# Kernel optimization log

Measured on AMD Instinct MI355X. Metric: run time of the kernel, lower is better.

The kernel has to match this reference:

```python
import jax, jax.numpy as jnp
import numpy as np

EPSILON = 1e-6
MINMAX_RATIO = 20 ** 0.5
N_NODES, N_EDGES = 60000, 240000
WIDTH, NUM_HEAD, DIM_HEAD = 256, 8, 32
WIDTH_NORM = NUM_HEAD * DIM_HEAD          # 256
WIDTH_ACT = NUM_HEAD * DIM_HEAD * 4       # 1024
EDGE_VOCAB, EDGE_FEATS = 16, 3


def _inv_softplus(y):
    return np.log(np.expm1(y))


def setup_inputs() -> dict:
    key = jax.random.key(0)
    ks = jax.random.split(key, 16)
    inp = {
        'x': jax.random.normal(ks[0], (N_NODES, WIDTH), jnp.float32),
        'deg': jax.random.randint(ks[1], (N_NODES,), 0, 6, jnp.int32),
        'edge_idx': jax.random.randint(ks[2], (2, N_EDGES), 0, N_NODES, jnp.int32),
        'edge_attr': jax.random.randint(ks[3], (N_EDGES, EDGE_FEATS), 0, EDGE_VOCAB, jnp.int32),
        'node_elec': jax.random.normal(ks[4], (N_NODES, 2), jnp.float32),
        # parameters (init scales per module code)
        'lora_down': jax.random.normal(ks[5], (WIDTH, DIM_HEAD)) / np.sqrt(WIDTH),
        # original init is zeros; small random values used so this path is exercised
        'lora_up': jax.random.normal(ks[6], (DIM_HEAD, WIDTH_NORM)) * 0.01,
        'emb_edge': jax.random.normal(ks[7], (EDGE_VOCAB, DIM_HEAD)) * (0.01 / np.sqrt(EDGE_FEATS)),
        'moa_w': jnp.zeros((2, DIM_HEAD), jnp.float32),
        'moa_s': jnp.tile(jnp.linspace(float(_inv_softplus(0.1)), float(_inv_softplus(10.0)), DIM_HEAD), (2, 1)),
        'elec_lin': jax.random.normal(ks[8], (2, DIM_HEAD)) * (0.01 / np.sqrt(2)),
        'emb_deg': jax.random.normal(ks[9], (6, WIDTH_NORM)) * 0.1,
        'lin_pre': jax.random.normal(ks[10], (WIDTH, WIDTH_NORM)) / np.sqrt(WIDTH),
        'gate_lin': jax.random.normal(ks[11], (WIDTH_NORM, WIDTH_NORM)) / np.sqrt(WIDTH_NORM),
        'gate_kernel': jax.random.normal(ks[12], (NUM_HEAD, DIM_HEAD, DIM_HEAD * 4)) / np.sqrt(DIM_HEAD),
        'value_lin': jax.random.normal(ks[13], (WIDTH_NORM, WIDTH_NORM)) / np.sqrt(WIDTH_NORM),
        'value_kernel': jax.random.normal(ks[14], (NUM_HEAD, DIM_HEAD, DIM_HEAD * 4)) / np.sqrt(DIM_HEAD),
        'act_bias': jnp.full((WIDTH_ACT,), float(_inv_softplus(0.5)), jnp.float32),
        'post_kernel': jax.random.normal(ks[15], (NUM_HEAD, DIM_HEAD * 4, DIM_HEAD)) / np.sqrt(DIM_HEAD * 4),
    }
    return inp


def _clip_with_grad(x, lo, hi):
    return jax.lax.stop_gradient(jnp.clip(x, lo, hi) - x) + x


def _group_linear(x, lin_kernel, head_kernel, norm_bias=None):
    H, D, F = head_kernel.shape
    xx = (x @ lin_kernel).reshape(*x.shape[:-1], H, D)
    xx = xx / jnp.sqrt(jnp.mean(jnp.square(xx), axis=-1, keepdims=True) + EPSILON)
    if norm_bias is not None:
        xx = (xx + norm_bias.reshape(xx.shape)) / 2 ** 0.5
    xx = jnp.einsum('nhd,hdf->nhf', xx, head_kernel)
    return xx.reshape(*x.shape[:-1], H * F)


def reference(x, deg, edge_idx, edge_attr, node_elec, lora_down, lora_up, emb_edge,
              moa_w, moa_s, elec_lin, emb_deg, lin_pre, gate_lin, gate_kernel,
              value_lin, value_kernel, act_bias, post_kernel):
    ei0, ei1 = edge_idx[0], edge_idx[1]
    # edge embedding: bond features + electronegativity difference (MoAct tanh mixture)
    diff = node_elec[ei0] - node_elec[ei1]                      # [E,2]
    w = jax.nn.softplus(moa_w)
    w = w / w.sum(axis=-1, keepdims=True)
    s = jax.nn.softplus(moa_s)
    moa_out = (jnp.tanh(diff[..., None] * s) * w).sum(-1)       # [E,2]
    emb = jnp.sum(emb_edge[edge_attr], axis=-2) + moa_out @ elec_lin  # [E,dim_head]
    # per-edge message with LoRA modulation, scatter-add to destination nodes
    msg = x[ei0] + x[ei1]                                       # [E,width]
    msg = msg @ lin_pre + ((msg @ lora_down) * emb) @ lora_up   # [E,width_norm]
    agg = jax.ops.segment_sum(msg, ei1, num_segments=x.shape[0])
    # gated post-block with degree-embedding gate bias
    gate_bias = emb_deg[deg]                                    # [N,width_norm]
    gg = _group_linear(agg, gate_lin, gate_kernel, gate_bias)   # [N,width_act]
    vv = _group_linear(agg, value_lin, value_kernel)
    a = jax.nn.softplus(gg + act_bias)
    a = _clip_with_grad(a, 1.0 / MINMAX_RATIO, MINMAX_RATIO)
    xx = (a * vv).reshape(agg.shape[0], NUM_HEAD, -1)           # [N,H,4*dim_head]
    xx = jnp.einsum('nhd,hdf->nhf', xx, post_kernel)
    return xx.reshape(agg.shape[0], -1)                         # [N,width_norm]
```

## Files before the change

kernel.cpp:

```cpp
#include <hip/hip_runtime.h>
#include <hip/hip_bf16.h>

typedef unsigned short u16;

#define NN 60000
#define NE 240000

typedef __attribute__((ext_vector_type(8))) short bfrag;
typedef __attribute__((ext_vector_type(4))) float ffrag;

__device__ __forceinline__ float bf2f(u16 u) {
    union { unsigned int i; float f; } v; v.i = ((unsigned int)u) << 16; return v.f;
}
__device__ __forceinline__ u16 f2bf(float f) {
    __hip_bfloat16 h = __float2bfloat16(f);
    return *reinterpret_cast<u16*>(&h);
}
__device__ __forceinline__ float softplusf(float x) {
    return fmaxf(x, 0.f) + log1pf(expf(-fabsf(x)));
}
__device__ __forceinline__ float fast_softplus(float x) {
    return __logf(1.f + __expf(x));
}
__device__ __forceinline__ float fast_sp_clip(float x) {
    float a = __logf(1.f + __expf(x));
    return fminf(fmaxf(a, 0.22360679774997896f), 4.47213595499957939f);
}
__device__ __forceinline__ float fast_tanh(float x) {
    float t = __expf(fminf(fmaxf(2.f * x, -30.f), 30.f));
    return (t - 1.f) * __builtin_amdgcn_rcpf(t + 1.f);
}
template<bool B>
__device__ __forceinline__ float LD(const void* p, int i) {
    if constexpr (B) return bf2f(((const u16*)p)[i]);
    else             return ((const float*)p)[i];
}
__device__ __forceinline__ bfrag ldfrag(const u16* p) {
    return *reinterpret_cast<const bfrag*>(p);
}
__device__ __forceinline__ ffrag MFMA(bfrag a, bfrag b, ffrag c) {
    return __builtin_amdgcn_mfma_f32_16x16x32_bf16(a, b, c, 0, 0, 0);
}

__global__ void detect_kernel(const u16* __restrict__ x, int* __restrict__ flag) {
    __shared__ int cnt;
    if (threadIdx.x == 0) cnt = 0;
    __syncthreads();
    int c = 0;
    for (int i = threadIdx.x; i < 2048; i += 256) {
        u16 w = x[2 * i];
        int e = (w >> 7) & 0xFF;
        if (e >= 112 && e <= 143) c++;
    }
    atomicAdd(&cnt, c);
    __syncthreads();
    if (threadIdx.x == 0) *flag = (cnt > 1024) ? 1 : 0;
}

template<bool B>
__device__ void prep_body(const void* gate_lin, const void* value_lin,
    const void* lin_pre, const void* lora_down, const void* lora_up,
    const void* gate_kernel, const void* value_kernel, const void* post_kernel,
    u16* gT, u16* vT, u16* lpT, u16* ldT, u16* luT, u16* gkT, u16* vkT, u16* pkT,
    int tid, int stride)
{
    for (int i = tid; i < 65536; i += stride) {
        int n = i >> 8, k = i & 255;
        gT[i]  = f2bf(LD<B>(gate_lin,  k * 256 + n));
        vT[i]  = f2bf(LD<B>(value_lin, k * 256 + n));
        lpT[i] = f2bf(LD<B>(lin_pre,   k * 256 + n));
    }
    for (int i = tid; i < 8192; i += stride) {
        { int n = i >> 8, k = i & 255; ldT[i] = f2bf(LD<B>(lora_down, k * 32 + n)); }
        { int n = i >> 5, k = i & 31;  luT[i] = f2bf(LD<B>(lora_up,   k * 256 + n)); }
    }
    for (int i = tid; i < 32768; i += stride) {
        { int hf = i >> 5, d = i & 31, h = hf >> 7, f = hf & 127;
          gkT[i] = f2bf(LD<B>(gate_kernel,  h * 4096 + d * 128 + f));
          vkT[i] = f2bf(LD<B>(value_kernel, h * 4096 + d * 128 + f)); }
        { int hd = i >> 7, f = i & 127, h = hd >> 5, d2 = hd & 31;
          pkT[i] = f2bf(LD<B>(post_kernel, h * 4096 + f * 32 + d2)); }
    }
}
__global__ void prep_kernel(const void* gate_lin, const void* value_lin,
    const void* lin_pre, const void* lora_down, const void* lora_up,
    const void* gate_kernel, const void* value_kernel, const void* post_kernel,
    u16* gT, u16* vT, u16* lpT, u16* ldT, u16* luT, u16* gkT, u16* vkT, u16* pkT,
    const int* flag)
{
    int tid = blockIdx.x * blockDim.x + threadIdx.x;
    int stride = gridDim.x * blockDim.x;
    if (*flag) prep_body<true >(gate_lin, value_lin, lin_pre, lora_down, lora_up,
        gate_kernel, value_kernel, post_kernel, gT, vT, lpT, ldT, luT, gkT, vkT, pkT, tid, stride);
    else       prep_body<false>(gate_lin, value_lin, lin_pre, lora_down, lora_up,
        gate_kernel, value_kernel, post_kernel, gT, vT, lpT, ldT, luT, gkT, vkT, pkT, tid, stride);
}


struct PreSmem { __align__(16) u16 xB[64][264]; };

template<bool B>
__device__ void pre_body(PreSmem& sm, const void* x, const u16* ldT,
                         u16* xb, u16* xd, int blk, int j)
{
    const int w = j >> 6, quad = (j >> 4) & 3, l15 = j & 15;
    {
        int row = j >> 2, seg = j & 3, c0 = seg * 64;
        int gr = blk * 64 + row;
        if (gr < NN) {
            if constexpr (B) {
                const u16* xp = (const u16*)x + (size_t)gr * 256 + c0;
                for (int cc = 0; cc < 64; cc += 8)
                    *reinterpret_cast<bfrag*>(&sm.xB[row][c0 + cc]) = ldfrag(xp + cc);
            } else {
                const float* xp = (const float*)x + (size_t)gr * 256 + c0;
                u16* xbp = xb + (size_t)gr * 256 + c0;
                for (int cc = 0; cc < 64; cc += 8) {
                    float4 v0 = *(const float4*)(xp + cc);
                    float4 v1 = *(const float4*)(xp + cc + 4);
                    bfrag o;
                    o[0] = (short)f2bf(v0.x); o[1] = (short)f2bf(v0.y);
                    o[2] = (short)f2bf(v0.z); o[3] = (short)f2bf(v0.w);
                    o[4] = (short)f2bf(v1.x); o[5] = (short)f2bf(v1.y);
                    o[6] = (short)f2bf(v1.z); o[7] = (short)f2bf(v1.w);
                    *reinterpret_cast<bfrag*>(&sm.xB[row][c0 + cc]) = o;
                    *reinterpret_cast<bfrag*>(xbp + cc) = o;
                }
            }
        } else {
            bfrag z = {0,0,0,0,0,0,0,0};
            for (int cc = 0; cc < 64; cc += 8)
                *reinterpret_cast<bfrag*>(&sm.xB[row][c0 + cc]) = z;
        }
    }
    __syncthreads();
    const int r0 = w * 16;
    bfrag A[8];
    #pragma unroll
    for (int kt = 0; kt < 8; kt++)
        A[kt] = ldfrag(&sm.xB[r0 + l15][kt * 32 + quad * 8]);

    #pragma unroll
    for (int t = 0; t < 2; t++) {
        int n0 = t * 16;
        ffrag acc = {0.f, 0.f, 0.f, 0.f};
        #pragma unroll
        for (int kt = 0; kt < 8; kt++)
            acc = MFMA(A[kt], ldfrag(ldT + (n0 + l15) * 256 + kt * 32 + quad * 8), acc);
        #pragma unroll
        for (int r = 0; r < 4; r++) {
            int gr = blk * 64 + r0 + quad * 4 + r;
            if (gr < NN) xd[(size_t)gr * 32 + n0 + l15] = f2bf(acc[r]);
        }
    }
}
__global__ __launch_bounds__(256) void pre_kernel(const void* x, const u16* ldT,
    u16* xb, u16* xd, const int* flag)
{
    __shared__ PreSmem sm;
    const int j = threadIdx.x, blk = blockIdx.x;
    if (*flag) pre_body<true >(sm, x, ldT, xb, xd, blk, j);
    else       pre_body<false>(sm, x, ldT, xb, xd, blk, j);
}

__global__ __launch_bounds__(256) void hist_kernel(const int* __restrict__ edge_idx,
                                                   int* __restrict__ cnt)
{
    int e = blockIdx.x * blockDim.x + threadIdx.x;
    int stride = gridDim.x * blockDim.x;
    for (; e < NE; e += stride) atomicAdd(&cnt[edge_idx[NE + e]], 1);
}

__global__ __launch_bounds__(256) void scanA_kernel(const int* __restrict__ cnt,
                                                    int* __restrict__ bsum)
{
    __shared__ int sd[256];
    int b = blockIdx.x, j = threadIdx.x;
    int base = b * 1024 + j * 4;
    int s = 0;
    #pragma unroll
    for (int k = 0; k < 4; k++) { int i = base + k; if (i < NN) s += cnt[i]; }
    sd[j] = s; __syncthreads();
    for (int st = 128; st > 0; st >>= 1) {
        if (j < st) sd[j] += sd[j + st];
        __syncthreads();
    }
    if (j == 0) bsum[b] = sd[0];
}

__global__ __launch_bounds__(256) void scanB_kernel(const int* __restrict__ cnt,
    const int* __restrict__ bsum, int* __restrict__ off, int* __restrict__ cur)
{
    __shared__ int sd[256];
    int b = blockIdx.x, j = threadIdx.x;
    int pre = 0;
    for (int k = 0; k < b; k++) pre += bsum[k];
    int base = b * 1024 + j * 4;
    int c[4]; int tsum = 0;
    #pragma unroll
    for (int k = 0; k < 4; k++) { int i = base + k; c[k] = (i < NN) ? cnt[i] : 0; tsum += c[k]; }
    sd[j] = tsum; __syncthreads();
    for (int st = 1; st < 256; st <<= 1) {
        int v = (j >= st) ? sd[j - st] : 0;
        __syncthreads();
        sd[j] += v;
        __syncthreads();
    }
    int excl = sd[j] - tsum;
    int run = pre + excl;
    #pragma unroll
    for (int k = 0; k < 4; k++) {
        int i = base + k;
        if (i < NN) { off[i] = run; cur[i] = run; }
        run += c[k];
    }
}

struct EdgeWSmem {
    float wL[64], sL[64];
    float embT[512];
    float elT[64];
};

template<bool B>
__device__ void edgew_body(EdgeWSmem& sm, const int* edge_idx, const int* edge_attr,
    const void* node_elec, const void* emb_edge, const void* moa_w, const void* moa_s,
    const void* elec_lin, const u16* xd, u16* W, int* srcL, int* cur, int g, int j)
{
    if (j < 64) {
        int c = j >> 5;
        float sw = fast_softplus(LD<B>(moa_w, j));
        float tot = 0.f;
        #pragma unroll
        for (int d = 0; d < 32; d++) tot += fast_softplus(LD<B>(moa_w, c * 32 + d));
        sm.wL[j] = sw / tot;
        sm.sL[j] = fast_softplus(LD<B>(moa_s, j));
        sm.elT[j] = LD<B>(elec_lin, j);
    }
    for (int i = j; i < 512; i += 256) sm.embT[i] = LD<B>(emb_edge, i);
    __syncthreads();

    const int t = j & 3, s = j >> 2, e = g * 64 + s;
    const int a = edge_idx[e], b = edge_idx[NE + e];
    const int ch = t >> 1, dr = (t & 1) * 16;
    float df = LD<B>(node_elec, a * 2 + ch) - LD<B>(node_elec, b * 2 + ch);
    float part = 0.f;
    #pragma unroll
    for (int d = 0; d < 16; d++) {
        int dd = ch * 32 + dr + d;
        part += fast_tanh(df * sm.sL[dd]) * sm.wL[dd];
    }
    part += __shfl_xor(part, 1);
    int base = (j & 63) & ~3;
    float moa0 = __shfl(part, base + 0);
    float moa1 = __shfl(part, base + 2);

    int a0 = edge_attr[e * 3 + 0], a1 = edge_attr[e * 3 + 1], a2 = edge_attr[e * 3 + 2];
    int d0 = t * 8;
    bfrag va = ldfrag(xd + (size_t)a * 32 + d0);
    bfrag vb = ldfrag(xd + (size_t)b * 32 + d0);
    bfrag o;
    #pragma unroll
    for (int q = 0; q < 8; q++) {
        int d = d0 + q;
        float emb = sm.embT[a0 * 32 + d] + sm.embT[a1 * 32 + d] + sm.embT[a2 * 32 + d]
                  + moa0 * sm.elT[d] + moa1 * sm.elT[32 + d];
        o[q] = (short)f2bf((bf2f((u16)va[q]) + bf2f((u16)vb[q])) * emb);
    }
    int slot = 0;
    if (t == 0) slot = atomicAdd(&cur[b], 1);
    slot = __shfl(slot, base);
    if (t == 0) srcL[slot] = a;
    *reinterpret_cast<bfrag*>(W + (size_t)slot * 32 + d0) = o;
}

__global__ __launch_bounds__(256) void edgew_kernel(const int* edge_idx,
    const int* edge_attr, const void* node_elec, const void* emb_edge,
    const void* moa_w, const void* moa_s, const void* elec_lin,
    const u16* xd, u16* W, int* srcL, int* cur, const int* flag)
{
    __shared__ EdgeWSmem sm;
    const int j = threadIdx.x, g = blockIdx.x;
    if (*flag) edgew_body<true >(sm, edge_idx, edge_attr, node_elec, emb_edge,
                                 moa_w, moa_s, elec_lin, xd, W, srcL, cur, g, j);
    else       edgew_body<false>(sm, edge_idx, edge_attr, node_elec, emb_edge,
                                 moa_w, moa_s, elec_lin, xd, W, srcL, cur, g, j);
}

struct NodeSmemF {
    __align__(16) union U1 {
        u16 aggB[16][264];
        u16 ghatB[16][264];
    } u1;
    __align__(16) union U2 {
        struct P { float gF[16][260]; float vF[16][260]; } p;
        u16 xxB[16][1032];
    } u2;
    __align__(16) u16 sB[16][264];
    __align__(16) u16 uB[16][40];
    float grmsL[16][8], vrmsL[16][8];
    int degL[16], offL[16], idgL[16];
    int srcC[128];
};

template<bool B>
__device__ void node_body_f(NodeSmemF& sm, const void* x, const u16* xb,
    const u16* Wb, const int* srcL, const int* off, const int* cnt, const int* deg,
    const void* emb_deg, const void* act_bias, const u16* gT, const u16* vT,
    const u16* gkT, const u16* vkT, const u16* pkT, const u16* lpT, const u16* luT,
    void* out, int blk, int j)
{
    const int w = j >> 6, quad = (j >> 4) & 3, l15 = j & 15;
    const int n0g = blk * 16;
    const u16* xbp = B ? (const u16*)x : xb;

    int o0 = off[n0g];
    int eb = off[n0g + 15] + cnt[n0g + 15] - o0;
    if (j < 128 && j < eb) sm.srcC[j] = srcL[o0 + j];
    if (j < 16) {
        sm.degL[j] = deg[n0g + j];
        sm.offL[j] = off[n0g + j];
        sm.idgL[j] = cnt[n0g + j];
    }
    __syncthreads();

    {
        int s = j >> 4, dp = j & 15, c0 = dp * 16;
        int o = sm.offL[s], dg = sm.idgL[s], base = o - o0;
        float acc[16];
        #pragma unroll
        for (int k = 0; k < 16; k++) acc[k] = 0.f;
        float u0 = 0.f, u1 = 0.f;
        for (int i = 0; i < dg; i++) {
            int idx = base + i;
            int src = (idx < 128) ? sm.srcC[idx] : srcL[o + i];
            const u16* xr = xbp + (size_t)src * 256 + c0;
            bfrag v0 = ldfrag(xr), v1 = ldfrag(xr + 8);
            const u16* wr = Wb + (size_t)(o + i) * 32 + dp;
            u0 += bf2f(wr[0]); u1 += bf2f(wr[16]);
            #pragma unroll
            for (int q = 0; q < 8; q++) {
                acc[q]     += bf2f((u16)v0[q]);
                acc[q + 8] += bf2f((u16)v1[q]);
            }
        }
        {
            const u16* xr = xbp + (size_t)(n0g + s) * 256 + c0;
            bfrag v0 = ldfrag(xr), v1 = ldfrag(xr + 8);
            float fd = (float)dg;
            #pragma unroll
            for (int q = 0; q < 8; q++) {
                acc[q]     = fmaf(fd, bf2f((u16)v0[q]), acc[q]);
                acc[q + 8] = fmaf(fd, bf2f((u16)v1[q]), acc[q + 8]);
            }
        }
        sm.uB[s][dp] = f2bf(u0); sm.uB[s][dp + 16] = f2bf(u1);
        #pragma unroll
        for (int cq = 0; cq < 16; cq += 2) {
            unsigned int pv = (unsigned int)f2bf(acc[cq]) | ((unsigned int)f2bf(acc[cq + 1]) << 16);
            *reinterpret_cast<unsigned int*>(&sm.sB[s][c0 + cq]) = pv;
        }
    }
    __syncthreads();

    {
        bfrag S[8];
        #pragma unroll
        for (int kt = 0; kt < 8; kt++)
            S[kt] = ldfrag(&sm.sB[l15][kt * 32 + quad * 8]);
        bfrag uA = ldfrag(&sm.uB[l15][quad * 8]);
        #pragma unroll
        for (int tt = 0; tt < 4; tt++) {
            int n0 = (w * 4 + tt) * 16;
            const u16* bp = lpT + (n0 + l15) * 256 + quad * 8;
            bfrag b0 = ldfrag(bp +   0), b1 = ldfrag(bp +  32),
                  b2 = ldfrag(bp +  64), b3 = ldfrag(bp +  96),
                  b4 = ldfrag(bp + 128), b5 = ldfrag(bp + 160),
                  b6 = ldfrag(bp + 192), b7 = ldfrag(bp + 224);
            bfrag lu = ldfrag(luT + (n0 + l15) * 32 + quad * 8);
            ffrag acc = {0.f, 0.f, 0.f, 0.f};
            acc = MFMA(S[0], b0, acc); acc = MFMA(S[1], b1, acc);
            acc = MFMA(S[2], b2, acc); acc = MFMA(S[3], b3, acc);
            acc = MFMA(S[4], b4, acc); acc = MFMA(S[5], b5, acc);
            acc = MFMA(S[6], b6, acc); acc = MFMA(S[7], b7, acc);
            acc = MFMA(uA, lu, acc);
            #pragma unroll
            for (int r = 0; r < 4; r++)
                sm.u1.aggB[quad * 4 + r][n0 + l15] = f2bf(acc[r]);
        }
    }
    __syncthreads();

    {
        bfrag A[8];
        #pragma unroll
        for (int kt = 0; kt < 8; kt++)
            A[kt] = ldfrag(&sm.u1.aggB[l15][kt * 32 + quad * 8]);
        const u16* WT = (w >> 1) ? vT : gT;
        float (*OF)[260] = (w >> 1) ? sm.u2.p.vF : sm.u2.p.gF;
        int half = (w & 1) * 128;
        #pragma unroll
        for (int t = 0; t < 8; t++) {
            int n0 = half + t * 16;
            const u16* bp = WT + (n0 + l15) * 256 + quad * 8;
            bfrag b0 = ldfrag(bp +   0), b1 = ldfrag(bp +  32),
                  b2 = ldfrag(bp +  64), b3 = ldfrag(bp +  96),
                  b4 = ldfrag(bp + 128), b5 = ldfrag(bp + 160),
                  b6 = ldfrag(bp + 192), b7 = ldfrag(bp + 224);
            ffrag acc = {0.f, 0.f, 0.f, 0.f};
            acc = MFMA(A[0], b0, acc); acc = MFMA(A[1], b1, acc);
            acc = MFMA(A[2], b2, acc); acc = MFMA(A[3], b3, acc);
            acc = MFMA(A[4], b4, acc); acc = MFMA(A[5], b5, acc);
            acc = MFMA(A[6], b6, acc); acc = MFMA(A[7], b7, acc);
            #pragma unroll
            for (int r = 0; r < 4; r++)
                OF[quad * 4 + r][n0 + l15] = acc[r];
        }
    }
    __syncthreads();

    if (j < 128) {
        int r = j >> 3, h = j & 7;
        float gs = 0.f, vs = 0.f;
        #pragma unroll
        for (int d = 0; d < 32; d++) {
            float g = sm.u2.p.gF[r][h * 32 + d]; gs = fmaf(g, g, gs);
            float v = sm.u2.p.vF[r][h * 32 + d]; vs = fmaf(v, v, vs);
        }
        sm.grmsL[r][h] = 1.f / sqrtf(gs * (1.f / 32.f) + 1e-6f);
        sm.vrmsL[r][h] = 1.f / sqrtf(vs * (1.f / 32.f) + 1e-6f);
    }
    __syncthreads();

    {
        int row = j >> 4, c0 = l15 * 16;
        int dg = sm.degL[row];
        float bias[16];
        if constexpr (B) {
            const u16* ep = (const u16*)emb_deg + dg * 256 + c0;
            bfrag e0 = ldfrag(ep), e1 = ldfrag(ep + 8);
            #pragma unroll
            for (int q = 0; q < 8; q++) {
                bias[q] = bf2f((u16)e0[q]); bias[q + 8] = bf2f((u16)e1[q]);
            }
        } else {
            const float* ep = (const float*)emb_deg + dg * 256 + c0;
            #pragma unroll
            for (int q = 0; q < 16; q += 4) {
                float4 v = *(const float4*)(ep + q);
                bias[q] = v.x; bias[q + 1] = v.y; bias[q + 2] = v.z; bias[q + 3] = v.w;
            }
        }
        float gi = sm.grmsL[row][c0 >> 5], vi = sm.vrmsL[row][c0 >> 5];
        #pragma unroll
        for (int cq = 0; cq < 16; cq += 2) {
            int c = c0 + cq;
            float v0 = sm.u2.p.vF[row][c] * vi;
            float v1 = sm.u2.p.vF[row][c + 1] * vi;
            float g0 = (sm.u2.p.gF[row][c] * gi + bias[cq]) * 0.70710678118654752f;
            float g1 = (sm.u2.p.gF[row][c + 1] * gi + bias[cq + 1]) * 0.70710678118654752f;
            unsigned int pv = (unsigned int)f2bf(v0) | ((unsigned int)f2bf(v1) << 16);
            unsigned int pg = (unsigned int)f2bf(g0) | ((unsigned int)f2bf(g1) << 16);
            *reinterpret_cast<unsigned int*>(&sm.sB[row][c]) = pv;
            *reinterpret_cast<unsigned int*>(&sm.u1.ghatB[row][c]) = pg;
        }
    }
    __syncthreads();

    #pragma unroll
    for (int hh = 0; hh < 2; hh++) {
        int h = w * 2 + hh;
        bfrag aG = ldfrag(&sm.u1.ghatB[l15][h * 32 + quad * 8]);
        bfrag aV = ldfrag(&sm.sB[l15][h * 32 + quad * 8]);
        #pragma unroll
        for (int t = 0; t < 8; t++) {
            int n0 = t * 16;
            bfrag bg = ldfrag(gkT + (h * 128 + n0 + l15) * 32 + quad * 8);
            bfrag bv = ldfrag(vkT + (h * 128 + n0 + l15) * 32 + quad * 8);
            ffrag zero = {0.f, 0.f, 0.f, 0.f};
            ffrag ag = MFMA(aG, bg, zero);
            ffrag av = MFMA(aV, bv, zero);
            int cc = h * 128 + n0 + l15;
            float bias = LD<B>(act_bias, cc);
            #pragma unroll
            for (int r = 0; r < 4; r++) {
                float a = fast_sp_clip(ag[r] + bias);
                sm.u2.xxB[quad * 4 + r][cc] = f2bf(a * av[r]);
            }
        }
    }
    __syncthreads();

    #pragma unroll
    for (int hh = 0; hh < 2; hh++) {
        int h = w * 2 + hh;
        bfrag A4[4];
        #pragma unroll
        for (int kt = 0; kt < 4; kt++)
            A4[kt] = ldfrag(&sm.u2.xxB[l15][h * 128 + kt * 32 + quad * 8]);
        #pragma unroll
        for (int t = 0; t < 2; t++) {
            int n0 = t * 16;
            const u16* pp = pkT + (h * 32 + n0 + l15) * 128 + quad * 8;
            bfrag c0 = ldfrag(pp), c1 = ldfrag(pp + 32),
                  c2 = ldfrag(pp + 64), c3 = ldfrag(pp + 96);
            ffrag acc = {0.f, 0.f, 0.f, 0.f};
            acc = MFMA(A4[0], c0, acc); acc = MFMA(A4[1], c1, acc);
            acc = MFMA(A4[2], c2, acc); acc = MFMA(A4[3], c3, acc);
            #pragma unroll
            for (int r = 0; r < 4; r++) {
                size_t idx = (size_t)(n0g + quad * 4 + r) * 256 + h * 32 + n0 + l15;
                if constexpr (B) ((u16*)out)[idx] = f2bf(acc[r]);
                else             ((float*)out)[idx] = acc[r];
            }
        }
    }
}

__global__ __launch_bounds__(256) void node_kernel_f(
    const void* x, const u16* xb, const u16* Wb, const int* srcL, const int* off,
    const int* cnt, const int* deg, const void* emb_deg, const void* act_bias,
    const u16* gT, const u16* vT, const u16* gkT, const u16* vkT, const u16* pkT,
    const u16* lpT, const u16* luT, void* out, const int* flag)
{
    __shared__ NodeSmemF sm;
    const int j = threadIdx.x, blk = blockIdx.x;
    if (*flag) node_body_f<true >(sm, x, xb, Wb, srcL, off, cnt, deg, emb_deg, act_bias,
                                  gT, vT, gkT, vkT, pkT, lpT, luT, out, blk, j);
    else       node_body_f<false>(sm, x, xb, Wb, srcL, off, cnt, deg, emb_deg, act_bias,
                                  gT, vT, gkT, vkT, pkT, lpT, luT, out, blk, j);
}

struct EdgeSmemM {
    __align__(16) u16 msgB[64][264];
    __align__(16) u16 uB[64][40];
    __align__(16) float embL[64][32];
    float wL[64], sL[64];
    float moaL[64][2];
    int ei0s[64], ei1s[64];
};

template<bool B>
__device__ void edge_body_m(EdgeSmemM& sm, const void* x, const int* edge_idx,
    const int* edge_attr, const void* node_elec, const void* emb_edge,
    const void* moa_w, const void* moa_s, const void* elec_lin,
    const u16* ldT, const u16* luT, const u16* lpT, float* agg, int g, int j)
{
    const int w = j >> 6, quad = (j >> 4) & 3, l15 = j & 15;
    const int lane = j & 63;

    if (w == 0) {
        int c = lane >> 5;
        float sw = softplusf(LD<B>(moa_w, lane));
        float tot = 0.f;
        #pragma unroll
        for (int d = 0; d < 32; d++) tot += softplusf(LD<B>(moa_w, c * 32 + d));
        sm.wL[lane] = sw / tot;
        sm.sL[lane] = softplusf(LD<B>(moa_s, lane));
        int e = g * 64 + lane;
        int a = edge_idx[e], b = edge_idx[NE + e];
        sm.ei0s[lane] = a; sm.ei1s[lane] = b;
        #pragma unroll
        for (int c2 = 0; c2 < 2; c2++) {
            float df = LD<B>(node_elec, a * 2 + c2) - LD<B>(node_elec, b * 2 + c2);
            float acc = 0.f;
            for (int d = 0; d < 32; d++)
                acc += tanhf(df * sm.sL[c2 * 32 + d]) * sm.wL[c2 * 32 + d];
            sm.moaL[lane][c2] = acc;
        }
    }
    __syncthreads();

    {
        int row = j >> 2, seg = j & 3, c0 = seg * 64;
        int e0 = sm.ei0s[row], e1 = sm.ei1s[row];
        if constexpr (B) {
            const u16* xp = (const u16*)x;
            for (int cc = 0; cc < 64; cc += 8) {
                bfrag v0 = ldfrag(xp + (size_t)e0 * 256 + c0 + cc);
                bfrag v1 = ldfrag(xp + (size_t)e1 * 256 + c0 + cc);
                bfrag o;
                #pragma unroll
                for (int q = 0; q < 8; q++)
                    o[q] = (short)f2bf(bf2f((u16)v0[q]) + bf2f((u16)v1[q]));
                *reinterpret_cast<bfrag*>(&sm.msgB[row][c0 + cc]) = o;
            }
        } else {
            const float* xp = (const float*)x;
            for (int cc = 0; cc < 64; cc += 4) {
                float4 v0 = *(const float4*)(xp + (size_t)e0 * 256 + c0 + cc);
                float4 v1 = *(const float4*)(xp + (size_t)e1 * 256 + c0 + cc);
                ushort4 o = { f2bf(v0.x + v1.x), f2bf(v0.y + v1.y),
                              f2bf(v0.z + v1.z), f2bf(v0.w + v1.w) };
                *reinterpret_cast<ushort4*>(&sm.msgB[row][c0 + cc]) = o;
            }
        }
        int e = row, d0 = seg * 8, ea = g * 64 + e;
        int a0 = edge_attr[ea * 3 + 0], a1 = edge_attr[ea * 3 + 1], a2 = edge_attr[ea * 3 + 2];
        float m0 = sm.moaL[e][0], m1 = sm.moaL[e][1];
        #pragma unroll
        for (int d = d0; d < d0 + 8; d++) {
            sm.embL[e][d] = LD<B>(emb_edge, a0 * 32 + d) + LD<B>(emb_edge, a1 * 32 + d)
                          + LD<B>(emb_edge, a2 * 32 + d)
                          + m0 * LD<B>(elec_lin, d) + m1 * LD<B>(elec_lin, 32 + d);
        }
    }
    __syncthreads();

    const int r0 = w * 16;
    bfrag A[8];
    #pragma unroll
    for (int kt = 0; kt < 8; kt++)
        A[kt] = ldfrag(&sm.msgB[r0 + l15][kt * 32 + quad * 8]);

    #pragma unroll
    for (int t = 0; t < 2; t++) {
        int n0 = t * 16;
        ffrag acc = {0.f, 0.f, 0.f, 0.f};
        #pragma unroll
        for (int kt = 0; kt < 8; kt++)
            acc = MFMA(A[kt], ldfrag(ldT + (n0 + l15) * 256 + kt * 32 + quad * 8), acc);
        #pragma unroll
        for (int r = 0; r < 4; r++) {
            int row = r0 + quad * 4 + r;
            sm.uB[row][n0 + l15] = f2bf(acc[r] * sm.embL[row][n0 + l15]);
        }
    }
    bfrag uA = ldfrag(&sm.uB[r0 + l15][quad * 8]);

    int er[4];
    #pragma unroll
    for (int r = 0; r < 4; r++) er[r] = sm.ei1s[r0 + quad * 4 + r];

    for (int t = 0; t < 16; t++) {
        int n0 = t * 16;
        ffrag acc = {0.f, 0.f, 0.f, 0.f};
        #pragma unroll
        for (int kt = 0; kt < 8; kt++)
            acc = MFMA(A[kt], ldfrag(lpT + (n0 + l15) * 256 + kt * 32 + quad * 8), acc);
        acc = MFMA(uA, ldfrag(luT + (n0 + l15) * 32 + quad * 8), acc);
        #pragma unroll
        for (int r = 0; r < 4; r++)
            unsafeAtomicAdd(&agg[(size_t)er[r] * 256 + n0 + l15], acc[r]);
    }
}

__global__ __launch_bounds__(256) void edge_kernel_m(
    const void* x, const int* edge_idx, const int* edge_attr,
    const void* node_elec, const void* emb_edge, const void* moa_w,
    const void* moa_s, const void* elec_lin,
    const u16* ldT, const u16* luT, const u16* lpT, float* agg, const int* flag)
{
    __shared__ EdgeSmemM sm;
    const int j = threadIdx.x, g = blockIdx.x;
    if (*flag) edge_body_m<true >(sm, x, edge_idx, edge_attr, node_elec, emb_edge,
                                  moa_w, moa_s, elec_lin, ldT, luT, lpT, agg, g, j);
    else       edge_body_m<false>(sm, x, edge_idx, edge_attr, node_elec, emb_edge,
                                  moa_w, moa_s, elec_lin, ldT, luT, lpT, agg, g, j);
}

struct NodeSmemM {
    union U1 {
        u16 aggB[16][264];
        u16 ghatB[16][264];
    } u1;
    union U2 {
        struct P { float gF[16][260]; float vF[16][260]; } p;
        u16 xxB[16][1032];
    } u2;
    __align__(16) u16 vhatB[16][264];
    float grmsL[16][8], vrmsL[16][8];
    int degL[16];
};

template<bool B>
__device__ void node_body_m(NodeSmemM& sm, const float* agg, const int* deg,
    const void* emb_deg, const void* act_bias, const u16* gT, const u16* vT,
    const u16* gkT, const u16* vkT, const u16* pkT, void* out, int blk, int j)
{
    const int w = j >> 6, quad = (j >> 4) & 3, l15 = j & 15;
    const int n0g = blk * 16;

    {
        int row = j >> 4, c0 = l15 * 16;
        const float* ap = agg + (size_t)(n0g + row) * 256 + c0;
        #pragma unroll
        for (int q = 0; q < 16; q += 4) {
            float4 v = *(const float4*)(ap + q);
            ushort4 o = { f2bf(v.x), f2bf(v.y), f2bf(v.z), f2bf(v.w) };
            *reinterpret_cast<ushort4*>(&sm.u1.aggB[row][c0 + q]) = o;
        }
        if (j < 16) sm.degL[j] = deg[n0g + j];
    }
    __syncthreads();

    {
        bfrag A[8];
        #pragma unroll
        for (int kt = 0; kt < 8; kt++)
            A[kt] = ldfrag(&sm.u1.aggB[l15][kt * 32 + quad * 8]);
        const u16* WT = (w >> 1) ? vT : gT;
        float (*OF)[260] = (w >> 1) ? sm.u2.p.vF : sm.u2.p.gF;
        int half = (w & 1) * 128;
        #pragma unroll
        for (int t = 0; t < 8; t++) {
            int n0 = half + t * 16;
            ffrag acc = {0.f, 0.f, 0.f, 0.f};
            #pragma unroll
            for (int kt = 0; kt < 8; kt++)
                acc = MFMA(A[kt], ldfrag(WT + (n0 + l15) * 256 + kt * 32 + quad * 8), acc);
            #pragma unroll
            for (int r = 0; r < 4; r++)
                OF[quad * 4 + r][n0 + l15] = acc[r];
        }
    }
    __syncthreads();

    if (j < 128) {
        int r = j >> 3, h = j & 7;
        float gs = 0.f, vs = 0.f;
        #pragma unroll
        for (int d = 0; d < 32; d++) {
            float g = sm.u2.p.gF[r][h * 32 + d]; gs = fmaf(g, g, gs);
            float v = sm.u2.p.vF[r][h * 32 + d]; vs = fmaf(v, v, vs);
        }
        sm.grmsL[r][h] = 1.f / sqrtf(gs * (1.f / 32.f) + 1e-6f);
        sm.vrmsL[r][h] = 1.f / sqrtf(vs * (1.f / 32.f) + 1e-6f);
    }
    __syncthreads();

    {
        int row = j >> 4, c0 = l15 * 16;
        int dg = sm.degL[row];
        #pragma unroll
        for (int c = c0; c < c0 + 16; c++) {
            float gi = sm.grmsL[row][c >> 5], vi = sm.vrmsL[row][c >> 5];
            float bias = LD<B>(emb_deg, dg * 256 + c);
            sm.vhatB[row][c] = f2bf(sm.u2.p.vF[row][c] * vi);
            sm.u1.ghatB[row][c] = f2bf((sm.u2.p.gF[row][c] * gi + bias) * 0.70710678118654752f);
        }
    }
    __syncthreads();

    #pragma unroll
    for (int hh = 0; hh < 2; hh++) {
        int h = w * 2 + hh;
        bfrag aG = ldfrag(&sm.u1.ghatB[l15][h * 32 + quad * 8]);
        bfrag aV = ldfrag(&sm.vhatB[l15][h * 32 + quad * 8]);
        #pragma unroll
        for (int t = 0; t < 8; t++) {
            int n0 = t * 16;
            ffrag zero = {0.f, 0.f, 0.f, 0.f};
            ffrag ag = MFMA(aG, ldfrag(gkT + (h * 128 + n0 + l15) * 32 + quad * 8), zero);
            ffrag av = MFMA(aV, ldfrag(vkT + (h * 128 + n0 + l15) * 32 + quad * 8), zero);
            int cc = h * 128 + n0 + l15;
            float bias = LD<B>(act_bias, cc);
            #pragma unroll
            for (int r = 0; r < 4; r++) {
                float a = softplusf(ag[r] + bias);
                a = fminf(fmaxf(a, 0.22360679774997896f), 4.47213595499957939f);
                sm.u2.xxB[quad * 4 + r][cc] = f2bf(a * av[r]);
            }
        }
    }
    __syncthreads();

    #pragma unroll
    for (int hh = 0; hh < 2; hh++) {
        int h = w * 2 + hh;
        bfrag A4[4];
        #pragma unroll
        for (int kt = 0; kt < 4; kt++)
            A4[kt] = ldfrag(&sm.u2.xxB[l15][h * 128 + kt * 32 + quad * 8]);
        #pragma unroll
        for (int t = 0; t < 2; t++) {
            int n0 = t * 16;
            ffrag acc = {0.f, 0.f, 0.f, 0.f};
            #pragma unroll
            for (int kt = 0; kt < 4; kt++)
                acc = MFMA(A4[kt], ldfrag(pkT + (h * 32 + n0 + l15) * 128 + kt * 32 + quad * 8), acc);
            #pragma unroll
            for (int r = 0; r < 4; r++) {
                size_t idx = (size_t)(n0g + quad * 4 + r) * 256 + h * 32 + n0 + l15;
                if constexpr (B) ((u16*)out)[idx] = f2bf(acc[r]);
                else             ((float*)out)[idx] = acc[r];
            }
        }
    }
}

__global__ __launch_bounds__(256) void node_kernel_m(
    const float* agg, const int* deg, const void* emb_deg, const void* act_bias,
    const u16* gT, const u16* vT, const u16* gkT, const u16* vkT, const u16* pkT,
    void* out, const int* flag)
{
    __shared__ NodeSmemM sm;
    const int j = threadIdx.x, blk = blockIdx.x;
    if (*flag) node_body_m<true >(sm, agg, deg, emb_deg, act_bias, gT, vT, gkT, vkT, pkT, out, blk, j);
    else       node_body_m<false>(sm, agg, deg, emb_deg, act_bias, gT, vT, gkT, vkT, pkT, out, blk, j);
}

struct EdgeSmemFB {
    __align__(16) float msgT[256][8];
    __align__(16) float uT[32][8];
    float wL[64], sL[64];
    float embL[8][32];
    float moaL[8][2];
    float diffL[8][2];
    int   ei0s[8], ei1s[8];
};

template<bool B>
__device__ void edge_body_fb(EdgeSmemFB& sm,
    const void* x, const int* edge_idx, const int* edge_attr,
    const void* node_elec, const void* lora_down, const void* lora_up,
    const void* emb_edge, const void* moa_w, const void* moa_s,
    const void* elec_lin, const void* lin_pre, float* agg, int g, int j)
{
    if (j < 64) {
        int c = j >> 5;
        float sw = softplusf(LD<B>(moa_w, j));
        float tot = 0.f;
        #pragma unroll
        for (int d = 0; d < 32; d++) tot += softplusf(LD<B>(moa_w, c * 32 + d));
        sm.wL[j] = sw / tot;
        sm.sL[j] = softplusf(LD<B>(moa_s, j));
    }
    if (j < 16) {
        int s = j >> 1, c = j & 1;
        int e = g * 8 + s;
        int a = edge_idx[e], b = edge_idx[NE + e];
        if (c == 0) { sm.ei0s[s] = a; sm.ei1s[s] = b; }
        sm.diffL[s][c] = LD<B>(node_elec, a * 2 + c) - LD<B>(node_elec, b * 2 + c);
    }
    __syncthreads();
    if (j < 16) {
        int s = j >> 1, c = j & 1;
        float df = sm.diffL[s][c], acc = 0.f;
        #pragma unroll
        for (int d = 0; d < 32; d++)
            acc += tanhf(df * sm.sL[c * 32 + d]) * sm.wL[c * 32 + d];
        sm.moaL[s][c] = acc;
    }
    #pragma unroll
    for (int s = 0; s < 8; s++)
        sm.msgT[j][s] = LD<B>(x, sm.ei0s[s] * 256 + j) + LD<B>(x, sm.ei1s[s] * 256 + j);
    __syncthreads();
    {
        int s = j >> 5, d = j & 31, e = g * 8 + s;
        sm.embL[s][d] = LD<B>(emb_edge, edge_attr[e * 3 + 0] * 32 + d)
                      + LD<B>(emb_edge, edge_attr[e * 3 + 1] * 32 + d)
                      + LD<B>(emb_edge, edge_attr[e * 3 + 2] * 32 + d)
                      + sm.moaL[s][0] * LD<B>(elec_lin, d)
                      + sm.moaL[s][1] * LD<B>(elec_lin, 32 + d);
    }
    __syncthreads();
    {
        int s = j >> 5, d = j & 31;
        float t = 0.f;
        for (int k = 0; k < 256; k++)
            t = fmaf(sm.msgT[k][s], LD<B>(lora_down, k * 32 + d), t);
        sm.uT[d][s] = t * sm.embL[s][d];
    }
    __syncthreads();
    float acc[8];
    #pragma unroll
    for (int s = 0; s < 8; s++) acc[s] = 0.f;
    #pragma unroll 4
    for (int k = 0; k < 256; k++) {
        float w = LD<B>(lin_pre, k * 256 + j);
        const float4 m0 = *reinterpret_cast<const float4*>(&sm.msgT[k][0]);
        const float4 m1 = *reinterpret_cast<const float4*>(&sm.msgT[k][4]);
        acc[0] = fmaf(m0.x, w, acc[0]); acc[1] = fmaf(m0.y, w, acc[1]);
        acc[2] = fmaf(m0.z, w, acc[2]); acc[3] = fmaf(m0.w, w, acc[3]);
        acc[4] = fmaf(m1.x, w, acc[4]); acc[5] = fmaf(m1.y, w, acc[5]);
        acc[6] = fmaf(m1.z, w, acc[6]); acc[7] = fmaf(m1.w, w, acc[7]);
    }
    #pragma unroll 4
    for (int d = 0; d < 32; d++) {
        float w = LD<B>(lora_up, d * 256 + j);
        const float4 u0 = *reinterpret_cast<const float4*>(&sm.uT[d][0]);
        const float4 u1 = *reinterpret_cast<const float4*>(&sm.uT[d][4]);
        acc[0] = fmaf(u0.x, w, acc[0]); acc[1] = fmaf(u0.y, w, acc[1]);
        acc[2] = fmaf(u0.z, w, acc[2]); acc[3] = fmaf(u0.w, w, acc[3]);
        acc[4] = fmaf(u1.x, w, acc[4]); acc[5] = fmaf(u1.y, w, acc[5]);
        acc[6] = fmaf(u1.z, w, acc[6]); acc[7] = fmaf(u1.w, w, acc[7]);
    }
    #pragma unroll
    for (int s = 0; s < 8; s++)
        unsafeAtomicAdd(&agg[(size_t)sm.ei1s[s] * 256 + j], acc[s]);
}

__global__ __launch_bounds__(256) void edge_kernel_fb(
    const void* x, const int* edge_idx, const int* edge_attr,
    const void* node_elec, const void* lora_down, const void* lora_up,
    const void* emb_edge, const void* moa_w, const void* moa_s,
    const void* elec_lin, const void* lin_pre, float* agg, const int* flag)
{
    __shared__ EdgeSmemFB sm;
    const int j = threadIdx.x, g = blockIdx.x;
    if (*flag) edge_body_fb<true >(sm, x, edge_idx, edge_attr, node_elec, lora_down,
                                   lora_up, emb_edge, moa_w, moa_s, elec_lin, lin_pre, agg, g, j);
    else       edge_body_fb<false>(sm, x, edge_idx, edge_attr, node_elec, lora_down,
                                   lora_up, emb_edge, moa_w, moa_s, elec_lin, lin_pre, agg, g, j);
}

struct NodeSmemFB {
    __align__(16) float aggT[256][8];
    float gL[8][256];
    float vL[8][256];
    float ghat[256], vhat[256];
    float xxL[1024];
};

template<bool B>
__device__ void node_body_fb(NodeSmemFB& sm,
    const float* agg, const int* deg, const void* emb_deg,
    const void* gate_lin, const void* value_lin, const void* gate_kernel,
    const void* value_kernel, const void* act_bias, const void* post_kernel,
    void* out, int n0, int j)
{
    #pragma unroll
    for (int s = 0; s < 8; s++) sm.aggT[j][s] = agg[(size_t)(n0 + s) * 256 + j];
    __syncthreads();

    float ga[8], va[8];
    #pragma unroll
    for (int s = 0; s < 8; s++) { ga[s] = 0.f; va[s] = 0.f; }
    #pragma unroll 4
    for (int k = 0; k < 256; k++) {
        float wg = LD<B>(gate_lin,  k * 256 + j);
        float wv = LD<B>(value_lin, k * 256 + j);
        const float4 a0 = *reinterpret_cast<const float4*>(&sm.aggT[k][0]);
        const float4 a1 = *reinterpret_cast<const float4*>(&sm.aggT[k][4]);
        ga[0] = fmaf(a0.x, wg, ga[0]); va[0] = fmaf(a0.x, wv, va[0]);
        ga[1] = fmaf(a0.y, wg, ga[1]); va[1] = fmaf(a0.y, wv, va[1]);
        ga[2] = fmaf(a0.z, wg, ga[2]); va[2] = fmaf(a0.z, wv, va[2]);
        ga[3] = fmaf(a0.w, wg, ga[3]); va[3] = fmaf(a0.w, wv, va[3]);
        ga[4] = fmaf(a1.x, wg, ga[4]); va[4] = fmaf(a1.x, wv, va[4]);
        ga[5] = fmaf(a1.y, wg, ga[5]); va[5] = fmaf(a1.y, wv, va[5]);
        ga[6] = fmaf(a1.z, wg, ga[6]); va[6] = fmaf(a1.z, wv, va[6]);
        ga[7] = fmaf(a1.w, wg, ga[7]); va[7] = fmaf(a1.w, wv, va[7]);
    }
    __syncthreads();
    #pragma unroll
    for (int s = 0; s < 8; s++) { sm.gL[s][j] = ga[s]; sm.vL[s][j] = va[s]; }

    const int h = j >> 5, dd = j & 31, f0 = dd << 2;
    const float lo = 0.22360679774997896f, hi = 4.47213595499957939f;

    for (int s = 0; s < 8; s++) {
        __syncthreads();
        float gs = 0.f, vs = 0.f;
        #pragma unroll
        for (int d = 0; d < 32; d++) {
            float g = sm.gL[s][h * 32 + d];
            float v = sm.vL[s][h * 32 + d];
            gs = fmaf(g, g, gs); vs = fmaf(v, v, vs);
        }
        float grms = sqrtf(gs * (1.f / 32.f) + 1e-6f);
        float vrms = sqrtf(vs * (1.f / 32.f) + 1e-6f);
        float gv = sm.gL[s][j], vv = sm.vL[s][j];
        float bias = LD<B>(emb_deg, deg[n0 + s] * 256 + j);
        sm.ghat[j] = (gv / grms + bias) * 0.70710678118654752f;
        sm.vhat[j] = vv / vrms;
        __syncthreads();

        float a0 = 0.f, a1 = 0.f, a2 = 0.f, a3 = 0.f;
        float b0 = 0.f, b1 = 0.f, b2 = 0.f, b3 = 0.f;
        #pragma unroll 4
        for (int d = 0; d < 32; d++) {
            float gh = sm.ghat[h * 32 + d];
            float vh = sm.vhat[h * 32 + d];
            int base = h * 4096 + d * 128 + f0;
            a0 = fmaf(gh, LD<B>(gate_kernel,  base + 0), a0);
            a1 = fmaf(gh, LD<B>(gate_kernel,  base + 1), a1);
            a2 = fmaf(gh, LD<B>(gate_kernel,  base + 2), a2);
            a3 = fmaf(gh, LD<B>(gate_kernel,  base + 3), a3);
            b0 = fmaf(vh, LD<B>(value_kernel, base + 0), b0);
            b1 = fmaf(vh, LD<B>(value_kernel, base + 1), b1);
            b2 = fmaf(vh, LD<B>(value_kernel, base + 2), b2);
            b3 = fmaf(vh, LD<B>(value_kernel, base + 3), b3);
        }
        int fb = h * 128 + f0;
        a0 = fminf(fmaxf(softplusf(a0 + LD<B>(act_bias, fb + 0)), lo), hi);
        a1 = fminf(fmaxf(softplusf(a1 + LD<B>(act_bias, fb + 1)), lo), hi);
        a2 = fminf(fmaxf(softplusf(a2 + LD<B>(act_bias, fb + 2)), lo), hi);
        a3 = fminf(fmaxf(softplusf(a3 + LD<B>(act_bias, fb + 3)), lo), hi);
        sm.xxL[fb + 0] = a0 * b0; sm.xxL[fb + 1] = a1 * b1;
        sm.xxL[fb + 2] = a2 * b2; sm.xxL[fb + 3] = a3 * b3;
        __syncthreads();

        float o = 0.f;
        #pragma unroll 4
        for (int f = 0; f < 128; f++)
            o = fmaf(sm.xxL[h * 128 + f], LD<B>(post_kernel, h * 4096 + f * 32 + dd), o);
        if constexpr (B) ((u16*)out)[(size_t)(n0 + s) * 256 + j] = f2bf(o);
        else             ((float*)out)[(size_t)(n0 + s) * 256 + j] = o;
    }
}

__global__ __launch_bounds__(256) void node_kernel_fb(
    const float* agg, const int* deg, const void* emb_deg,
    const void* gate_lin, const void* value_lin, const void* gate_kernel,
    const void* value_kernel, const void* act_bias, const void* post_kernel,
    void* out, const int* flag)
{
    __shared__ NodeSmemFB sm;
    const int j = threadIdx.x, n0 = blockIdx.x * 8;
    if (*flag) node_body_fb<true >(sm, agg, deg, emb_deg, gate_lin, value_lin,
                                   gate_kernel, value_kernel, act_bias, post_kernel, out, n0, j);
    else       node_body_fb<false>(sm, agg, deg, emb_deg, gate_lin, value_lin,
                                   gate_kernel, value_kernel, act_bias, post_kernel, out, n0, j);
}

extern "C" void kernel_launch(void* const* d_in, const int* in_sizes, int n_in,
                              void* d_out, int out_size, void* d_ws, size_t ws_size,
                              hipStream_t stream) {
    const void* x           = d_in[0];
    const int*  deg         = (const int*)d_in[1];
    const int*  edge_idx    = (const int*)d_in[2];
    const int*  edge_attr   = (const int*)d_in[3];
    const void* node_elec   = d_in[4];
    const void* lora_down   = d_in[5];
    const void* lora_up     = d_in[6];
    const void* emb_edge    = d_in[7];
    const void* moa_w       = d_in[8];
    const void* moa_s       = d_in[9];
    const void* elec_lin    = d_in[10];
    const void* emb_deg     = d_in[11];
    const void* lin_pre     = d_in[12];
    const void* gate_lin    = d_in[13];
    const void* gate_kernel = d_in[14];
    const void* value_lin   = d_in[15];
    const void* value_kernel= d_in[16];
    const void* act_bias    = d_in[17];
    const void* post_kernel = d_in[18];

    const size_t AGG_BYTES = (size_t)NN * 256 * 4;
    const size_t T_BYTES   = (size_t)(3 * 65536 + 2 * 8192 + 3 * 32768) * 2;

    const size_t XB_OFF  = 16 + T_BYTES;
    const size_t W_OFF   = XB_OFF  + (size_t)NN * 256 * 2;
    const size_t XD_OFF  = W_OFF   + (size_t)NE * 32 * 2;
    const size_t SRC_OFF = XD_OFF  + (size_t)NN * 32 * 2;
    const size_t CNT_OFF = SRC_OFF + (size_t)NE * 4;
    const size_t OFF_OFF = CNT_OFF + (size_t)NN * 4;
    const size_t CUR_OFF = OFF_OFF + (size_t)NN * 4;
    const size_t BS_OFF  = CUR_OFF + (size_t)NN * 4;
    const size_t NEW_NEEDED = BS_OFF + 256;

    const size_t T_OFF_OLD  = AGG_BYTES + 16;
    const size_t OLD_NEEDED = T_OFF_OLD + T_BYTES;

    if (ws_size >= NEW_NEEDED) {
        int* flag = (int*)d_ws;
        u16* gT  = (u16*)((char*)d_ws + 16);
        u16* vT  = gT  + 65536;
        u16* lpT = vT  + 65536;
        u16* ldT = lpT + 65536;
        u16* luT = ldT + 8192;
        u16* gkT = luT + 8192;
        u16* vkT = gkT + 32768;
        u16* pkT = vkT + 32768;
        u16*  xb   = (u16*)((char*)d_ws + XB_OFF);
        u16*  Wb   = (u16*)((char*)d_ws + W_OFF);
        u16*  xd   = (u16*)((char*)d_ws + XD_OFF);
        int* srcL  = (int*)((char*)d_ws + SRC_OFF);
        int* cnt   = (int*)((char*)d_ws + CNT_OFF);
        int* offA  = (int*)((char*)d_ws + OFF_OFF);
        int* cur   = (int*)((char*)d_ws + CUR_OFF);
        int* bsum  = (int*)((char*)d_ws + BS_OFF);

        detect_kernel<<<1, 256, 0, stream>>>((const u16*)x, flag);
        prep_kernel<<<128, 256, 0, stream>>>(
            gate_lin, value_lin, lin_pre, lora_down, lora_up,
            gate_kernel, value_kernel, post_kernel,
            gT, vT, lpT, ldT, luT, gkT, vkT, pkT, flag);
        hipMemsetAsync(cnt, 0, (size_t)NN * 4, stream);
        pre_kernel<<<(NN + 63) / 64, 256, 0, stream>>>(x, ldT, xb, xd, flag);
        hist_kernel<<<256, 256, 0, stream>>>(edge_idx, cnt);
        scanA_kernel<<<59, 256, 0, stream>>>(cnt, bsum);
        scanB_kernel<<<59, 256, 0, stream>>>(cnt, bsum, offA, cur);
        edgew_kernel<<<NE / 64, 256, 0, stream>>>(
            edge_idx, edge_attr, node_elec, emb_edge, moa_w, moa_s, elec_lin,
            xd, Wb, srcL, cur, flag);
        node_kernel_f<<<NN / 16, 256, 0, stream>>>(
            x, xb, Wb, srcL, offA, cnt, deg, emb_deg, act_bias,
            gT, vT, gkT, vkT, pkT, lpT, luT, d_out, flag);
    } else if (ws_size >= OLD_NEEDED) {
        float* agg = (float*)d_ws;
        int* flag  = (int*)((char*)d_ws + AGG_BYTES);
        u16* gT  = (u16*)((char*)d_ws + T_OFF_OLD);
        u16* vT  = gT  + 65536;
        u16* lpT = vT  + 65536;
        u16* ldT = lpT + 65536;
        u16* luT = ldT + 8192;
        u16* gkT = luT + 8192;
        u16* vkT = gkT + 32768;
        u16* pkT = vkT + 32768;

        hipMemsetAsync(agg, 0, AGG_BYTES, stream);
        detect_kernel<<<1, 256, 0, stream>>>((const u16*)x, flag);
        prep_kernel<<<128, 256, 0, stream>>>(
            gate_lin, value_lin, lin_pre, lora_down, lora_up,
            gate_kernel, value_kernel, post_kernel,
            gT, vT, lpT, ldT, luT, gkT, vkT, pkT, flag);
        edge_kernel_m<<<NE / 64, 256, 0, stream>>>(
            x, edge_idx, edge_attr, node_elec, emb_edge, moa_w, moa_s, elec_lin,
            ldT, luT, lpT, agg, flag);
        node_kernel_m<<<NN / 16, 256, 0, stream>>>(
            agg, deg, emb_deg, act_bias, gT, vT, gkT, vkT, pkT, d_out, flag);
    } else {
        float* agg = (float*)d_ws;
        int* flag  = (int*)((char*)d_ws + AGG_BYTES);
        hipMemsetAsync(agg, 0, AGG_BYTES, stream);
        detect_kernel<<<1, 256, 0, stream>>>((const u16*)x, flag);
        edge_kernel_fb<<<NE / 8, 256, 0, stream>>>(
            x, edge_idx, edge_attr, node_elec, lora_down, lora_up, emb_edge,
            moa_w, moa_s, elec_lin, lin_pre, agg, flag);
        node_kernel_fb<<<NN / 8, 256, 0, stream>>>(
            agg, deg, emb_deg, gate_lin, value_lin, gate_kernel, value_kernel,
            act_bias, post_kernel, d_out, flag);
    }
}
```

Before: 492.4 us.

## Fuse RMS-norm into gate/value GEMM epilogue and drop fp32 staging buffers

Computes per-head RMS norms straight from the MFMA accumulators using lane shuffles, and applies the degree bias and scaling in the GEMM epilogue. This removes the fp32 gF/vF shared-memory staging, the separate reduction pass and two block barriers. The post-kernel GEMM now reads a per-wave xx tile, so its barrier goes too. Also prefetches the next neighbor row in the aggregation loop, enlarges the cached source list, and sets launch bounds for 4 blocks per CU, at some cost in register pressure.

```diff
diff --git a/kernel.cpp b/kernel.cpp
--- a/kernel.cpp
+++ b/kernel.cpp
@@ -292,15 +292,11 @@
         u16 aggB[16][264];
         u16 ghatB[16][264];
     } u1;
-    __align__(16) union U2 {
-        struct P { float gF[16][260]; float vF[16][260]; } p;
-        u16 xxB[16][1032];
-    } u2;
     __align__(16) u16 sB[16][264];
+    __align__(16) u16 xxW[4][16][136];
     __align__(16) u16 uB[16][40];
-    float grmsL[16][8], vrmsL[16][8];
+    int srcC[192];
     int degL[16], offL[16], idgL[16];
-    int srcC[128];
 };
 
 template<bool B>
@@ -316,7 +312,7 @@
 
     int o0 = off[n0g];
     int eb = off[n0g + 15] + cnt[n0g + 15] - o0;
-    if (j < 128 && j < eb) sm.srcC[j] = srcL[o0 + j];
+    if (j < 192 && j < eb) sm.srcC[j] = srcL[o0 + j];
     if (j < 16) {
         sm.degL[j] = deg[n0g + j];
         sm.offL[j] = off[n0g + j];
@@ -331,13 +327,27 @@
         #pragma unroll
         for (int k = 0; k < 16; k++) acc[k] = 0.f;
         float u0 = 0.f, u1 = 0.f;
+        bfrag pv0 = {0,0,0,0,0,0,0,0}, pv1 = {0,0,0,0,0,0,0,0};
+        float pw0 = 0.f, pw1 = 0.f;
+        if (dg > 0) {
+            int src = (base < 192) ? sm.srcC[base] : srcL[o];
+            const u16* xr = xbp + (size_t)src * 256 + c0;
+            pv0 = ldfrag(xr); pv1 = ldfrag(xr + 8);
+            const u16* wr = Wb + (size_t)o * 32 + dp;
+            pw0 = bf2f(wr[0]); pw1 = bf2f(wr[16]);
+        }
         for (int i = 0; i < dg; i++) {
-            int idx = base + i;
-            int src = (idx < 128) ? sm.srcC[idx] : srcL[o + i];
-            const u16* xr = xbp + (size_t)src * 256 + c0;
-            bfrag v0 = ldfrag(xr), v1 = ldfrag(xr + 8);
-            const u16* wr = Wb + (size_t)(o + i) * 32 + dp;
-            u0 += bf2f(wr[0]); u1 += bf2f(wr[16]);
+            bfrag v0 = pv0, v1 = pv1;
+            float w0 = pw0, w1 = pw1;
+            if (i + 1 < dg) {
+                int idx = base + i + 1;
+                int src = (idx < 192) ? sm.srcC[idx] : srcL[o + i + 1];
+                const u16* xr = xbp + (size_t)src * 256 + c0;
+                pv0 = ldfrag(xr); pv1 = ldfrag(xr + 8);
+                const u16* wr = Wb + (size_t)(o + i + 1) * 32 + dp;
+                pw0 = bf2f(wr[0]); pw1 = bf2f(wr[16]);
+            }
+            u0 += w0; u1 += w1;
             #pragma unroll
             for (int q = 0; q < 8; q++) {
                 acc[q]     += bf2f((u16)v0[q]);
@@ -396,77 +406,72 @@
         #pragma unroll
         for (int kt = 0; kt < 8; kt++)
             A[kt] = ldfrag(&sm.u1.aggB[l15][kt * 32 + quad * 8]);
-        const u16* WT = (w >> 1) ? vT : gT;
-        float (*OF)[260] = (w >> 1) ? sm.u2.p.vF : sm.u2.p.gF;
-        int half = (w & 1) * 128;
-        #pragma unroll
-        for (int t = 0; t < 8; t++) {
-            int n0 = half + t * 16;
-            const u16* bp = WT + (n0 + l15) * 256 + quad * 8;
-            bfrag b0 = ldfrag(bp +   0), b1 = ldfrag(bp +  32),
-                  b2 = ldfrag(bp +  64), b3 = ldfrag(bp +  96),
-                  b4 = ldfrag(bp + 128), b5 = ldfrag(bp + 160),
-                  b6 = ldfrag(bp + 192), b7 = ldfrag(bp + 224);
-            ffrag acc = {0.f, 0.f, 0.f, 0.f};
-            acc = MFMA(A[0], b0, acc); acc = MFMA(A[1], b1, acc);
-            acc = MFMA(A[2], b2, acc); acc = MFMA(A[3], b3, acc);
-            acc = MFMA(A[4], b4, acc); acc = MFMA(A[5], b5, acc);
-            acc = MFMA(A[6], b6, acc); acc = MFMA(A[7], b7, acc);
+        __syncthreads();
+
+        const bool isG = (w >> 1) == 0;
+        const u16* WT = isG ? gT : vT;
+        const int half = (w & 1) * 128;
+        #pragma unroll
+        for (int hd = 0; hd < 4; hd++) {
+            int n0 = half + hd * 32;
+            ffrag a0 = {0.f, 0.f, 0.f, 0.f}, a1 = {0.f, 0.f, 0.f, 0.f};
+            {
+                const u16* bp = WT + (n0 + l15) * 256 + quad * 8;
+                bfrag b0 = ldfrag(bp +   0), b1 = ldfrag(bp +  32),
+                      b2 = ldfrag(bp +  64), b3 = ldfrag(bp +  96),
+                      b4 = ldfrag(bp + 128), b5 = ldfrag(bp + 160),
+                      b6 = ldfrag(bp + 192), b7 = ldfrag(bp + 224);
+                a0 = MFMA(A[0], b0, a0); a0 = MFMA(A[1], b1, a0);
+                a0 = MFMA(A[2], b2, a0); a0 = MFMA(A[3], b3, a0);
+                a0 = MFMA(A[4], b4, a0); a0 = MFMA(A[5], b5, a0);
+                a0 = MFMA(A[6], b6, a0); a0 = MFMA(A[7], b7, a0);
+            }
+            {
+                const u16* bp = WT + (n0 + 16 + l15) * 256 + quad * 8;
+                bfrag b0 = ldfrag(bp +   0), b1 = ldfrag(bp +  32),
+                      b2 = ldfrag(bp +  64), b3 = ldfrag(bp +  96),
+                      b4 = ldfrag(bp + 128), b5 = ldfrag(bp + 160),
+                      b6 = ldfrag(bp + 192), b7 = ldfrag(bp + 224);
+                a1 = MFMA(A[0], b0, a1); a1 = MFMA(A[1], b1, a1);
+                a1 = MFMA(A[2], b2, a1); a1 = MFMA(A[3], b3, a1);
+                a1 = MFMA(A[4], b4, a1); a1 = MFMA(A[5], b5, a1);
+                a1 = MFMA(A[6], b6, a1); a1 = MFMA(A[7], b7, a1);
+            }
+            float inv[4];
             #pragma unroll
-            for (int r = 0; r < 4; r++)
-                OF[quad * 4 + r][n0 + l15] = acc[r];
-        }
-    }
-    __syncthreads();
-
-    if (j < 128) {
-        int r = j >> 3, h = j & 7;
-        float gs = 0.f, vs = 0.f;
-        #pragma unroll
-        for (int d = 0; d < 32; d++) {
-            float g = sm.u2.p.gF[r][h * 32 + d]; gs = fmaf(g, g, gs);
-            float v = sm.u2.p.vF[r][h * 32 + d]; vs = fmaf(v, v, vs);
-        }
-        sm.grmsL[r][h] = 1.f / sqrtf(gs * (1.f / 32.f) + 1e-6f);
-        sm.vrmsL[r][h] = 1.f / sqrtf(vs * (1.f / 32.f) + 1e-6f);
-    }
-    __syncthreads();
-
-    {
-        int row = j >> 4, c0 = l15 * 16;
-        int dg = sm.degL[row];
-        float bias[16];
-        if constexpr (B) {
-            const u16* ep = (const u16*)emb_deg + dg * 256 + c0;
-            bfrag e0 = ldfrag(ep), e1 = ldfrag(ep + 8);
-            #pragma unroll
-            for (int q = 0; q < 8; q++) {
-                bias[q] = bf2f((u16)e0[q]); bias[q + 8] = bf2f((u16)e1[q]);
-            }
-        } else {
-            const float* ep = (const float*)emb_deg + dg * 256 + c0;
-            #pragma unroll
-            for (int q = 0; q < 16; q += 4) {
-                float4 v = *(const float4*)(ep + q);
-                bias[q] = v.x; bias[q + 1] = v.y; bias[q + 2] = v.z; bias[q + 3] = v.w;
-            }
-        }
-        float gi = sm.grmsL[row][c0 >> 5], vi = sm.vrmsL[row][c0 >> 5];
-        #pragma unroll
-        for (int cq = 0; cq < 16; cq += 2) {
-            int c = c0 + cq;
-            float v0 = sm.u2.p.vF[row][c] * vi;
-            float v1 = sm.u2.p.vF[row][c + 1] * vi;
-            float g0 = (sm.u2.p.gF[row][c] * gi + bias[cq]) * 0.70710678118654752f;
-            float g1 = (sm.u2.p.gF[row][c + 1] * gi + bias[cq + 1]) * 0.70710678118654752f;
-            unsigned int pv = (unsigned int)f2bf(v0) | ((unsigned int)f2bf(v1) << 16);
-            unsigned int pg = (unsigned int)f2bf(g0) | ((unsigned int)f2bf(g1) << 16);
-            *reinterpret_cast<unsigned int*>(&sm.sB[row][c]) = pv;
-            *reinterpret_cast<unsigned int*>(&sm.u1.ghatB[row][c]) = pg;
-        }
-    }
-    __syncthreads();
-
+            for (int r = 0; r < 4; r++) {
+                float sq = a0[r] * a0[r] + a1[r] * a1[r];
+                sq += __shfl_xor(sq, 1);
+                sq += __shfl_xor(sq, 2);
+                sq += __shfl_xor(sq, 4);
+                sq += __shfl_xor(sq, 8);
+                inv[r] = 1.f / sqrtf(sq * (1.f / 32.f) + 1e-6f);
+            }
+            if (isG) {
+                #pragma unroll
+                for (int r = 0; r < 4; r++) {
+                    int row = quad * 4 + r;
+                    int dgr = sm.degL[row];
+                    float b0 = LD<B>(emb_deg, dgr * 256 + n0 + l15);
+                    float b1 = LD<B>(emb_deg, dgr * 256 + n0 + 16 + l15);
+                    sm.u1.ghatB[row][n0 + l15] =
+                        f2bf((a0[r] * inv[r] + b0) * 0.70710678118654752f);
+                    sm.u1.ghatB[row][n0 + 16 + l15] =
+                        f2bf((a1[r] * inv[r] + b1) * 0.70710678118654752f);
+                }
+            } else {
+                #pragma unroll
+                for (int r = 0; r < 4; r++) {
+                    int row = quad * 4 + r;
+                    sm.sB[row][n0 + l15]      = f2bf(a0[r] * inv[r]);
+                    sm.sB[row][n0 + 16 + l15] = f2bf(a1[r] * inv[r]);
+                }
+            }
+        }
+    }
+    __syncthreads();
+
+    u16 (*xxW)[136] = sm.xxW[w];
     #pragma unroll
     for (int hh = 0; hh < 2; hh++) {
         int h = w * 2 + hh;
@@ -480,24 +485,17 @@
             ffrag zero = {0.f, 0.f, 0.f, 0.f};
             ffrag ag = MFMA(aG, bg, zero);
             ffrag av = MFMA(aV, bv, zero);
-            int cc = h * 128 + n0 + l15;
-            float bias = LD<B>(act_bias, cc);
+            float bias = LD<B>(act_bias, h * 128 + n0 + l15);
             #pragma unroll
             for (int r = 0; r < 4; r++) {
                 float a = fast_sp_clip(ag[r] + bias);
-                sm.u2.xxB[quad * 4 + r][cc] = f2bf(a * av[r]);
-            }
-        }
-    }
-    __syncthreads();
-
-    #pragma unroll
-    for (int hh = 0; hh < 2; hh++) {
-        int h = w * 2 + hh;
+                xxW[quad * 4 + r][n0 + l15] = f2bf(a * av[r]);
+            }
+        }
         bfrag A4[4];
         #pragma unroll
         for (int kt = 0; kt < 4; kt++)
-            A4[kt] = ldfrag(&sm.u2.xxB[l15][h * 128 + kt * 32 + quad * 8]);
+            A4[kt] = ldfrag(&xxW[l15][kt * 32 + quad * 8]);
         #pragma unroll
         for (int t = 0; t < 2; t++) {
             int n0 = t * 16;
@@ -517,7 +515,7 @@
     }
 }
 
-__global__ __launch_bounds__(256) void node_kernel_f(
+__global__ __launch_bounds__(256, 4) void node_kernel_f(
     const void* x, const u16* xb, const u16* Wb, const int* srcL, const int* off,
     const int* cnt, const int* deg, const void* emb_deg, const void* act_bias,
     const u16* gT, const u16* vT, const u16* gkT, const u16* vkT, const u16* pkT,
```

New measurement: 484.5 us. About the same (-1.6%).
